# Performance work log

Hardware: AMD Instinct MI355X
Metric: run time of the kernel (lower is better)

## Reference

```python
import jax, jax.numpy as jnp
import numpy as np

B = 512      # batch of scenes
K = 16       # entities (slots) per scene
H = 500      # h == HIDDEN_SIZE (required by fc2 input width 2*HIDDEN_SIZE)
A = 64       # action_size
EPS = 1e-5


def layernorm(x, g, b):
    mu = jnp.mean(x, axis=-1, keepdims=True)
    var = jnp.var(x, axis=-1, keepdims=True)
    return (x - mu) * jax.lax.rsqrt(var + EPS) * g + b


def setup_inputs() -> dict:
    key = jax.random.key(0)
    ks = jax.random.split(key, 40)
    def W(i, shape, scale=0.02):
        return (jax.random.normal(ks[i], shape, dtype=jnp.float32) * scale)
    inp = {
        "state": jax.random.normal(ks[0], (B * K, H), dtype=jnp.float32),
        "actions": jax.random.normal(ks[1], (B, A), dtype=jnp.float32),
        # action path
        "ac_fc1_w": W(2, (A, H)), "ac_fc1_b": jnp.zeros((H,), jnp.float32),
        "ac_ln1_g": jnp.ones((H,), jnp.float32), "ac_ln1_b": jnp.zeros((H,), jnp.float32),
        "ac_fc2_w": W(3, (2 * H, H)), "ac_fc2_b": jnp.zeros((H,), jnp.float32),
        "ac_lnf2_w": W(4, (H, H)), "ac_lnf2_b": jnp.zeros((H,), jnp.float32),  # ac_ln_f2 is a Linear in the source
        "ac_fc3_w": W(5, (2 * H, 1)), "ac_fc3_b": jnp.zeros((1,), jnp.float32),
        # main path
        "fc1_w": W(6, (H, H)), "fc1_b": jnp.zeros((H,), jnp.float32),
        "ln1_g": jnp.ones((H,), jnp.float32), "ln1_b": jnp.zeros((H,), jnp.float32),
        "fc2_w": W(7, (2 * H, H)), "fc2_b": jnp.zeros((H,), jnp.float32),
        "ln2_g": jnp.ones((H,), jnp.float32), "ln2_b": jnp.zeros((H,), jnp.float32),
        "fc3_w": W(8, (H, H)), "fc3_b": jnp.zeros((H,), jnp.float32),
        "ln3_g": jnp.ones((H,), jnp.float32), "ln3_b": jnp.zeros((H,), jnp.float32),
        "fc4_w": W(9, (H, 100)), "fc4_b": jnp.zeros((100,), jnp.float32),
        "ln4_g": jnp.ones((100,), jnp.float32), "ln4_b": jnp.zeros((100,), jnp.float32),
        "fc5_w": W(10, (100, 1)), "fc5_b": jnp.zeros((1,), jnp.float32),
        "fc6_w": W(11, (2 * H, H)), "fc6_b": jnp.zeros((H,), jnp.float32),
        "ln6_g": jnp.ones((H,), jnp.float32), "ln6_b": jnp.zeros((H,), jnp.float32),
    }
    return inp


def reference(state, actions,
              ac_fc1_w, ac_fc1_b, ac_ln1_g, ac_ln1_b,
              ac_fc2_w, ac_fc2_b, ac_lnf2_w, ac_lnf2_b, ac_fc3_w, ac_fc3_b,
              fc1_w, fc1_b, ln1_g, ln1_b,
              fc2_w, fc2_b, ln2_g, ln2_b,
              fc3_w, fc3_b, ln3_g, ln3_b,
              fc4_w, fc4_b, ln4_g, ln4_b,
              fc5_w, fc5_b,
              fc6_w, fc6_b, ln6_g, ln6_b):
    b, k, h, nc = B, K, H, K - 1

    # ---- action_forward (has_action=True) ----
    a = layernorm(actions @ ac_fc1_w + ac_fc1_b, ac_ln1_g, ac_ln1_b)      # [b, h]
    a = jnp.broadcast_to(a[:, None, :], (b, k, h)).reshape(b * k, h)       # repeat over k
    concat_a = jnp.concatenate([state, a], axis=1)                          # [b*k, 2h]
    attention_a = jax.nn.sigmoid(concat_a @ ac_fc3_w + ac_fc3_b)           # [b*k, 1]
    effect = (concat_a @ ac_fc2_w + ac_fc2_b) @ ac_lnf2_w + ac_lnf2_b      # ac_ln_f2 is Linear
    state = effect * attention_a                                            # [b*k, h]

    # ---- per-entity encoder ----
    s1 = jax.nn.relu(layernorm(state @ fc1_w + fc1_b, ln1_g, ln1_b))       # [b*k, h]
    s1r = s1.reshape(b, k, h)

    # ---- all-pairs context gather: for each i, all j != i ----
    idx = np.array([[j for j in range(k) if j != i] for i in range(k)])    # [k, k-1] static
    cs = s1r[:, idx, :]                                                     # [b, k, k-1, h]
    fs = jnp.broadcast_to(s1r[:, :, None, :], (b, k, nc, h))               # [b, k, k-1, h]
    pair = jnp.concatenate([fs, cs], axis=-1).reshape(b * k * nc, 2 * h)   # [b*k*(k-1), 2h]

    # ---- edge MLP ----
    core = jax.nn.relu(layernorm(pair @ fc2_w + fc2_b, ln2_g, ln2_b))      # [b*k*nc, h]
    context = jax.nn.relu(layernorm(core @ fc3_w + fc3_b, ln3_g, ln3_b))
    context = context.reshape(b * k, nc, h)

    # ---- attention-weighted sum aggregation ----
    att = jnp.tanh(layernorm(core @ fc4_w + fc4_b, ln4_g, ln4_b))          # [b*k*nc, 100]
    att = jax.nn.sigmoid(att @ fc5_w + fc5_b).reshape(b * k, nc, 1)
    effect_sum = jnp.sum(context * att, axis=1)                             # [b*k, h]

    # ---- update ----
    total = jnp.concatenate([s1, effect_sum], axis=1)                       # [b*k, 2h]
    h_new = layernorm(total @ fc6_w + fc6_b, ln6_g, ln6_b)                  # [b*k, h]
    return h_new
```

## Files before the change

### kernel.cpp

```cpp
#include <hip/hip_runtime.h>
#include <math.h>


#define EPSF 1e-5f
typedef unsigned short u16;
typedef unsigned int u32;

typedef __bf16 bf16x8 __attribute__((ext_vector_type(8)));
typedef float f32x4 __attribute__((ext_vector_type(4)));
typedef u16 u16x8 __attribute__((ext_vector_type(8)));

__device__ __forceinline__ float bf2f(u16 u) {
  return __builtin_bit_cast(float, (u32)u << 16);
}
__device__ __forceinline__ u16 f2bf(float f) {
  u32 u = __builtin_bit_cast(u32, f);
  return (u16)((u + 0x7FFFu + ((u >> 16) & 1u)) >> 16);
}

#define GLOAD16(g, l) __builtin_amdgcn_global_load_lds( \
    (__attribute__((address_space(1))) u32*)(g), \
    (__attribute__((address_space(3))) u32*)(l), 16, 0, 0)

template <typename TOUT>
__global__ __launch_bounds__(256) void gemm_mfma(
    const u16* __restrict__ A, const u16* __restrict__ A2,
    const u16* __restrict__ Bt,
    const float* __restrict__ bias, const float* __restrict__ rowscale,
    TOUT* __restrict__ C, int M, int Npad, int K, int lda, int khalf)
{
  __shared__ __align__(16) u16 As[2][128 * 64];
  __shared__ __align__(16) u16 Bs[2][64 * 64];
  const int tid = threadIdx.x;
  const int lane = tid & 63, wid = tid >> 6;

  const int ncols = gridDim.x;
  const int nwg = ncols * gridDim.y;
  const int bid = blockIdx.y * ncols + blockIdx.x;
  const int swz = (bid & 7) * (nwg >> 3) + (bid >> 3);
  const size_t row0 = (size_t)(swz / ncols) * 128;
  const size_t col0 = (size_t)(swz % ncols) * 64;

  f32x4 acc[2][4] = {};

  const int s_sub = tid >> 3;
  const int s_chunk = (tid & 7) ^ (s_sub & 7);
  const size_t aoff = (row0 + s_sub) * (size_t)lda + s_chunk * 8;
  const u16* gA = A + aoff;
  const u16* gA2 = A2 ? (A2 + aoff - khalf) : nullptr;
  const u16* gB = Bt + (col0 + s_sub) * (size_t)K + s_chunk * 8;

  const int fr = lane & 15, fq = lane >> 4;
  const int cx0 = fq ^ (fr & 7);
  const int cx1 = (4 + fq) ^ (fr & 7);

  const int nkt = K >> 6;
  int cur = 0;

  {
#pragma unroll
    for (int h = 0; h < 4; ++h)
      GLOAD16(gA + (size_t)h * 32 * lda, &As[0][(h * 256 + tid) * 8]);
#pragma unroll
    for (int h = 0; h < 2; ++h)
      GLOAD16(gB + (size_t)h * 32 * K, &Bs[0][(h * 256 + tid) * 8]);
  }

  for (int kt = 0; kt < nkt; ++kt) {
    if (kt + 1 < nkt) {
      const int kk = (kt + 1) * 64;
      const u16* a = (A2 && kk >= khalf) ? (gA2 + kk) : (gA + kk);
      const u16* b = gB + kk;
#pragma unroll
      for (int h = 0; h < 4; ++h)
        GLOAD16(a + (size_t)h * 32 * lda, &As[cur ^ 1][(h * 256 + tid) * 8]);
#pragma unroll
      for (int h = 0; h < 2; ++h)
        GLOAD16(b + (size_t)h * 32 * K, &Bs[cur ^ 1][(h * 256 + tid) * 8]);
      asm volatile("s_waitcnt vmcnt(6)" ::: "memory");
    } else {
      asm volatile("s_waitcnt vmcnt(0)" ::: "memory");
    }
    __builtin_amdgcn_sched_barrier(0);
    __builtin_amdgcn_s_barrier();
    __builtin_amdgcn_sched_barrier(0);

    const u16* as = As[cur];
    const u16* bs = Bs[cur];
#pragma unroll
    for (int ks = 0; ks < 2; ++ks) {
      const int cx = ks ? cx1 : cx0;
      bf16x8 af[2], bf[4];
#pragma unroll
      for (int m = 0; m < 2; ++m) {
        int row = wid * 32 + m * 16 + fr;
        af[m] = *reinterpret_cast<const bf16x8*>(as + (row * 8 + cx) * 8);
      }
#pragma unroll
      for (int n = 0; n < 4; ++n) {
        int row = n * 16 + fr;
        bf[n] = *reinterpret_cast<const bf16x8*>(bs + (row * 8 + cx) * 8);
      }
#pragma unroll
      for (int m = 0; m < 2; ++m)
#pragma unroll
        for (int n = 0; n < 4; ++n)
          acc[m][n] = __builtin_amdgcn_mfma_f32_16x16x32_bf16(af[m], bf[n], acc[m][n], 0, 0, 0);
    }
    asm volatile("s_waitcnt lgkmcnt(0)" ::: "memory");
    __builtin_amdgcn_sched_barrier(0);
    __builtin_amdgcn_s_barrier();
    __builtin_amdgcn_sched_barrier(0);
    cur ^= 1;
  }

  const int cl = lane & 15, rg = lane >> 4;
#pragma unroll
  for (int m = 0; m < 2; ++m) {
#pragma unroll
    for (int n = 0; n < 4; ++n) {
      size_t col = col0 + n * 16 + cl;
      float bv = bias[col];
#pragma unroll
      for (int r = 0; r < 4; ++r) {
        size_t row = row0 + wid * 32 + m * 16 + rg * 4 + r;
        float v = acc[m][n][r] + bv;
        if (rowscale) v *= rowscale[row];
        if constexpr (sizeof(TOUT) == 2) C[row * Npad + col] = f2bf(v);
        else                             C[row * Npad + col] = v;
      }
    }
  }
}

__global__ __launch_bounds__(256) void gemm128(
    const float* __restrict__ A, const float* __restrict__ B,
    const float* __restrict__ bias, float* __restrict__ C, int M, int N, int K)
{
  __shared__ float As[16][132];
  __shared__ float Bs[16][128];
  const int tid = threadIdx.x;
  const int tx = tid & 15, ty = tid >> 4;
  const int row0 = blockIdx.y * 128, col0 = blockIdx.x * 128;
  float acc[8][8];
#pragma unroll
  for (int i = 0; i < 8; ++i)
#pragma unroll
    for (int j = 0; j < 8; ++j) acc[i][j] = 0.f;

  const int nkt = (K + 15) >> 4;
  for (int kt = 0; kt < nkt; ++kt) {
    const int k0 = kt << 4;
#pragma unroll
    for (int h = 0; h < 2; ++h) {
      int i = tid + h * 256;
      int m = i >> 2, kk = (i & 3) << 2;
      int gm = row0 + m, gk = k0 + kk;
      float4 v = make_float4(0.f, 0.f, 0.f, 0.f);
      if (gm < M && gk < K) v = *reinterpret_cast<const float4*>(A + (size_t)gm * K + gk);
      As[kk + 0][m] = v.x; As[kk + 1][m] = v.y; As[kk + 2][m] = v.z; As[kk + 3][m] = v.w;
    }
#pragma unroll
    for (int h = 0; h < 2; ++h) {
      int i = tid + h * 256;
      int kk = i >> 5, n = (i & 31) << 2;
      int gk = k0 + kk, gn = col0 + n;
      float4 v = make_float4(0.f, 0.f, 0.f, 0.f);
      if (gk < K && gn < N) v = *reinterpret_cast<const float4*>(B + (size_t)gk * N + gn);
      *reinterpret_cast<float4*>(&Bs[kk][n]) = v;
    }
    __syncthreads();
#pragma unroll
    for (int kk = 0; kk < 16; ++kk) {
      float4 a0 = *reinterpret_cast<const float4*>(&As[kk][ty * 4]);
      float4 a1 = *reinterpret_cast<const float4*>(&As[kk][ty * 4 + 64]);
      float4 b0 = *reinterpret_cast<const float4*>(&Bs[kk][tx * 4]);
      float4 b1 = *reinterpret_cast<const float4*>(&Bs[kk][tx * 4 + 64]);
      float av[8] = {a0.x, a0.y, a0.z, a0.w, a1.x, a1.y, a1.z, a1.w};
      float bv[8] = {b0.x, b0.y, b0.z, b0.w, b1.x, b1.y, b1.z, b1.w};
#pragma unroll
      for (int i = 0; i < 8; ++i)
#pragma unroll
        for (int j = 0; j < 8; ++j) acc[i][j] += av[i] * bv[j];
    }
    __syncthreads();
  }
#pragma unroll
  for (int i = 0; i < 8; ++i) {
    int gm = row0 + ty * 4 + ((i >> 2) << 6) + (i & 3);
    if (gm >= M) continue;
#pragma unroll
    for (int j = 0; j < 8; ++j) {
      int gn = col0 + tx * 4 + ((j >> 2) << 6) + (j & 3);
      if (gn < N) C[(size_t)gm * N + gn] = acc[i][j] + bias[gn];
    }
  }
}

template <int ACT, typename TIN, typename TOUT>
__global__ __launch_bounds__(256) void ln_wave4(
    const TIN* __restrict__ X, TOUT* __restrict__ Y,
    const float* __restrict__ g, const float* __restrict__ b,
    int ldx, int ldy)
{
  int w = threadIdx.x >> 6, lane = threadIdx.x & 63;
  int id0 = (blockIdx.x * 4 + w) * 4;
  int k0 = lane * 8;
  float xv[4][8], s[4], s2[4];
#pragma unroll
  for (int r = 0; r < 4; ++r) {
    s[r] = 0.f; s2[r] = 0.f;
    if constexpr (sizeof(TIN) == 2) {
      u16x8 u = *reinterpret_cast<const u16x8*>((const u16*)X + (size_t)(id0 + r) * ldx + k0);
#pragma unroll
      for (int e = 0; e < 8; ++e) xv[r][e] = bf2f(u[e]);
    } else {
      const float* x = (const float*)X + (size_t)(id0 + r) * ldx;
      if (k0 + 8 <= 500) {
        float4 a = *reinterpret_cast<const float4*>(x + k0);
        float4 c = *reinterpret_cast<const float4*>(x + k0 + 4);
        xv[r][0] = a.x; xv[r][1] = a.y; xv[r][2] = a.z; xv[r][3] = a.w;
        xv[r][4] = c.x; xv[r][5] = c.y; xv[r][6] = c.z; xv[r][7] = c.w;
      } else {
#pragma unroll
        for (int e = 0; e < 8; ++e) xv[r][e] = (k0 + e < 500) ? x[k0 + e] : 0.f;
      }
    }
#pragma unroll
    for (int e = 0; e < 8; ++e) { s[r] += xv[r][e]; s2[r] += xv[r][e] * xv[r][e]; }
  }
#pragma unroll
  for (int m = 32; m; m >>= 1)
#pragma unroll
    for (int r = 0; r < 4; ++r) {
      s[r] += __shfl_xor(s[r], m);
      s2[r] += __shfl_xor(s2[r], m);
    }
  float gv[8], bv[8];
#pragma unroll
  for (int e = 0; e < 8; ++e) {
    int k = k0 + e;
    gv[e] = (k < 500) ? g[k] : 0.f;
    bv[e] = (k < 500) ? b[k] : 0.f;
  }
#pragma unroll
  for (int r = 0; r < 4; ++r) {
    float mu = s[r] / 500.f;
    float rstd = rsqrtf(s2[r] / 500.f - mu * mu + EPSF);
    float ov[8];
#pragma unroll
    for (int e = 0; e < 8; ++e) {
      float v = (k0 + e < 500) ? ((xv[r][e] - mu) * rstd * gv[e] + bv[e]) : 0.f;
      if (ACT == 1) v = fmaxf(v, 0.f);
      ov[e] = v;
    }
    if constexpr (sizeof(TOUT) == 2) {
      u16x8 o;
#pragma unroll
      for (int e = 0; e < 8; ++e) o[e] = f2bf(ov[e]);
      *reinterpret_cast<u16x8*>((u16*)Y + (size_t)(id0 + r) * ldy + k0) = o;
    } else {
      float* y = (float*)Y + (size_t)(id0 + r) * ldy;
      if (k0 + 4 <= 500)
        *reinterpret_cast<float4*>(y + k0) = make_float4(ov[0], ov[1], ov[2], ov[3]);
      if (k0 + 8 <= 500)
        *reinterpret_cast<float4*>(y + k0 + 4) = make_float4(ov[4], ov[5], ov[6], ov[7]);
    }
  }
}

__global__ __launch_bounds__(256) void build_concat(
    const float* __restrict__ state, const u16* __restrict__ a, u16* __restrict__ cat)
{
  int r = blockIdx.x, t = threadIdx.x;
  int b = r >> 4;
  u16* c = cat + (size_t)r * 1024;
  if (t < 125) {
    float4 v = *reinterpret_cast<const float4*>(state + (size_t)r * 500 + t * 4);
    ushort4 o; o.x = f2bf(v.x); o.y = f2bf(v.y); o.z = f2bf(v.z); o.w = f2bf(v.w);
    *reinterpret_cast<ushort4*>(c + t * 4) = o;
    *reinterpret_cast<ushort4*>(c + 500 + t * 4) =
        *reinterpret_cast<const ushort4*>(a + (size_t)b * 512 + t * 4);
  }
  if (t < 24) c[1000 + t] = 0;
}

__global__ __launch_bounds__(256) void dot_sig4(
    const u16* __restrict__ cat, const float* __restrict__ w3,
    const float* __restrict__ b3, float* __restrict__ atta)
{
  int w = threadIdx.x >> 6, lane = threadIdx.x & 63;
  int r0 = (blockIdx.x * 4 + w) * 4;
  int k0 = lane * 16;
  float wv[16];
#pragma unroll
  for (int e = 0; e < 16; ++e) wv[e] = (k0 + e < 1000) ? w3[k0 + e] : 0.f;
  float s[4];
#pragma unroll
  for (int r = 0; r < 4; ++r) {
    const u16* x = cat + (size_t)(r0 + r) * 1024 + k0;
    u16x8 u0 = *reinterpret_cast<const u16x8*>(x);
    u16x8 u1 = *reinterpret_cast<const u16x8*>(x + 8);
    float acc = 0.f;
#pragma unroll
    for (int e = 0; e < 8; ++e) acc += bf2f(u0[e]) * wv[e];
#pragma unroll
    for (int e = 0; e < 8; ++e) acc += bf2f(u1[e]) * wv[8 + e];
    s[r] = acc;
  }
#pragma unroll
  for (int m = 32; m; m >>= 1)
#pragma unroll
    for (int r = 0; r < 4; ++r) s[r] += __shfl_xor(s[r], m);
  if (lane == 0) {
#pragma unroll
    for (int r = 0; r < 4; ++r)
      atta[r0 + r] = 1.f / (1.f + expf(-(s[r] + b3[0])));
  }
}

__global__ __launch_bounds__(256) void core_build3(
    const u16* __restrict__ PQ, u16* __restrict__ core,
    const float* __restrict__ g2, const float* __restrict__ b2, int c0)
{
  int w = threadIdx.x >> 6, lane = threadIdx.x & 63;
  int id0 = (blockIdx.x * 4 + w) * 4;
  int k0 = lane * 8;
  u16x8 up[4], uq[4];
#pragma unroll
  for (int r = 0; r < 4; ++r) {
    int id = id0 + r;
    int pp = id / 15, j = id - pp * 15;
    int gp = c0 + pp, i = gp & 15;
    int col = j + (j >= i);
    int r2 = (gp & ~15) | col;
    up[r] = *reinterpret_cast<const u16x8*>(PQ + (size_t)gp * 1024 + k0);
    uq[r] = *reinterpret_cast<const u16x8*>(PQ + (size_t)r2 * 1024 + 512 + k0);
  }
  float xv[4][8], s[4], s2[4];
#pragma unroll
  for (int r = 0; r < 4; ++r) {
    s[r] = 0.f; s2[r] = 0.f;
#pragma unroll
    for (int e = 0; e < 8; ++e) {
      float v = bf2f(up[r][e]) + bf2f(uq[r][e]);
      xv[r][e] = v; s[r] += v; s2[r] += v * v;
    }
  }
#pragma unroll
  for (int m = 32; m; m >>= 1)
#pragma unroll
    for (int r = 0; r < 4; ++r) {
      s[r] += __shfl_xor(s[r], m);
      s2[r] += __shfl_xor(s2[r], m);
    }
  float gv[8], bv[8];
#pragma unroll
  for (int e = 0; e < 8; ++e) {
    int k = k0 + e;
    gv[e] = (k < 500) ? g2[k] : 0.f;
    bv[e] = (k < 500) ? b2[k] : 0.f;
  }
#pragma unroll
  for (int r = 0; r < 4; ++r) {
    float mu = s[r] / 500.f;
    float rstd = rsqrtf(s2[r] / 500.f - mu * mu + EPSF);
    u16x8 o;
#pragma unroll
    for (int e = 0; e < 8; ++e)
      o[e] = (k0 + e < 500) ? f2bf(fmaxf((xv[r][e] - mu) * rstd * gv[e] + bv[e], 0.f)) : (u16)0;
    *reinterpret_cast<u16x8*>(core + (size_t)(id0 + r) * 512 + k0) = o;
  }
}

__global__ __launch_bounds__(256) void chunk_post3(
    const u16* __restrict__ V,
    const float* __restrict__ g3, const float* __restrict__ b3,
    const float* __restrict__ g4, const float* __restrict__ b4,
    const float* __restrict__ w5, const float* __restrict__ b5,
    u16* __restrict__ esum16, int c0)
{
  __shared__ u16 rows[15][512];
  __shared__ float st[15][4];
  int pp = blockIdx.x, t = threadIdx.x;
  int lane = t & 63, w = t >> 6;
  int k0 = lane * 8;
  int kk = lane * 2;

  u16x8 u[4]; ushort2 ua[4];
#pragma unroll
  for (int r = 0; r < 4; ++r) {
    int j = w * 4 + r;
    if (j < 15) {
      const u16* vr = V + (size_t)(pp * 15 + j) * 640;
      u[r] = *reinterpret_cast<const u16x8*>(vr + k0);
      ua[r] = *reinterpret_cast<const ushort2*>(vr + 512 + kk);
    }
  }
  float s[4], s2[4], sa[4], sa2[4], y0[4], y1[4];
#pragma unroll
  for (int r = 0; r < 4; ++r) {
    s[r] = s2[r] = sa[r] = sa2[r] = 0.f; y0[r] = y1[r] = 0.f;
    int j = w * 4 + r;
    if (j < 15) {
#pragma unroll
      for (int e = 0; e < 8; ++e) { float v = bf2f(u[r][e]); s[r] += v; s2[r] += v * v; }
      y0[r] = bf2f(ua[r].x); y1[r] = bf2f(ua[r].y);
      sa[r] = y0[r] + y1[r]; sa2[r] = y0[r] * y0[r] + y1[r] * y1[r];
      *reinterpret_cast<u16x8*>(&rows[j][k0]) = u[r];
    }
  }
#pragma unroll
  for (int m = 32; m; m >>= 1)
#pragma unroll
    for (int r = 0; r < 4; ++r) {
      s[r]   += __shfl_xor(s[r], m);
      s2[r]  += __shfl_xor(s2[r], m);
      sa[r]  += __shfl_xor(sa[r], m);
      sa2[r] += __shfl_xor(sa2[r], m);
    }
  float dv[4];
#pragma unroll
  for (int r = 0; r < 4; ++r) {
    float mu4 = sa[r] / 100.f;
    float rstd4 = rsqrtf(sa2[r] / 100.f - mu4 * mu4 + EPSF);
    float d = 0.f;
    if (kk < 100)     d += tanhf((y0[r] - mu4) * rstd4 * g4[kk] + b4[kk]) * w5[kk];
    if (kk + 1 < 100) d += tanhf((y1[r] - mu4) * rstd4 * g4[kk + 1] + b4[kk + 1]) * w5[kk + 1];
    dv[r] = d;
  }
#pragma unroll
  for (int m = 32; m; m >>= 1)
#pragma unroll
    for (int r = 0; r < 4; ++r) dv[r] += __shfl_xor(dv[r], m);
  if (lane == 0) {
#pragma unroll
    for (int r = 0; r < 4; ++r) {
      int j = w * 4 + r;
      if (j < 15) {
        float mu = s[r] / 500.f;
        st[j][0] = mu;
        st[j][1] = rsqrtf(s2[r] / 500.f - mu * mu + EPSF);
        st[j][2] = 1.f / (1.f + expf(-(dv[r] + b5[0])));
      }
    }
  }
  __syncthreads();

  u16* o = esum16 + (size_t)(c0 + pp) * 512;
  for (int n = t; n < 500; n += 256) {
    float gg = g3[n], bb = b3[n], acc = 0.f;
#pragma unroll
    for (int j = 0; j < 15; ++j) {
      float v = bf2f(rows[j][n]);
      acc += fmaxf((v - st[j][0]) * st[j][1] * gg + bb, 0.f) * st[j][2];
    }
    o[n] = f2bf(acc);
  }
  if (t < 12) o[500 + t] = 0;
}

struct TJob {
  const float* src; u16* dst;
  int K, N, srcLd, ldDst, nOff, kOff, tileBase, tilesX;
};
struct TJobs { TJob j[9]; int total; };

__global__ void pack_weights(TJobs jobs)
{
  __shared__ float tl[32][33];
  int bid = blockIdx.x;
  int ji = 0;
#pragma unroll
  for (int q = 1; q < 9; ++q) if (bid >= jobs.j[q].tileBase) ji = q;
  const TJob& J = jobs.j[ji];
  int t = bid - J.tileBase;
  int bx = t % J.tilesX, by = t / J.tilesX;
  int tx = threadIdx.x, ty = threadIdx.y;
  int k0 = by * 32, n0 = bx * 32;
#pragma unroll
  for (int r = 0; r < 4; ++r) {
    int row = k0 + ty + r * 8;
    if (row < J.K && n0 + tx < J.N) tl[ty + r * 8][tx] = J.src[(size_t)row * J.srcLd + n0 + tx];
  }
  __syncthreads();
#pragma unroll
  for (int r = 0; r < 4; ++r) {
    int n = n0 + ty + r * 8, k = k0 + tx;
    if (n < J.N && k < J.K)
      J.dst[(size_t)(n + J.nOff) * J.ldDst + J.kOff + k] = f2bf(tl[tx][ty + r * 8]);
  }
}

__global__ void pack_biases(
    const float* ac2, const float* lnf2, const float* f1, const float* f2,
    const float* f3, const float* f4, const float* f6,
    float* b_ac2p, float* b_lnf2p, float* b_f1p, float* b2p, float* b34p, float* b_f6p)
{
  int t = threadIdx.x;
  switch (blockIdx.x) {
    case 0: if (t < 512) b_ac2p[t]  = (t < 500) ? ac2[t]  : 0.f; break;
    case 1: if (t < 512) b_lnf2p[t] = (t < 500) ? lnf2[t] : 0.f; break;
    case 2: if (t < 512) b_f1p[t]   = (t < 500) ? f1[t]   : 0.f; break;
    case 3: b2p[t] = (t < 500) ? f2[t] : 0.f; break;
    case 4: if (t < 640) b34p[t] = (t < 500) ? f3[t] : ((t >= 512 && t < 612) ? f4[t - 512] : 0.f); break;
    case 5: if (t < 512) b_f6p[t]   = (t < 500) ? f6[t]   : 0.f; break;
  }
}

extern "C" void kernel_launch(void* const* d_in, const int* in_sizes, int n_in,
                              void* d_out, int out_size, void* d_ws, size_t ws_size,
                              hipStream_t stream)
{
  const float* state    = (const float*)d_in[0];
  const float* actions  = (const float*)d_in[1];
  const float* ac_fc1_w = (const float*)d_in[2];
  const float* ac_fc1_b = (const float*)d_in[3];
  const float* ac_ln1_g = (const float*)d_in[4];
  const float* ac_ln1_b = (const float*)d_in[5];
  const float* ac_fc2_w = (const float*)d_in[6];
  const float* ac_fc2_b = (const float*)d_in[7];
  const float* ac_lnf2_w= (const float*)d_in[8];
  const float* ac_lnf2_b= (const float*)d_in[9];
  const float* ac_fc3_w = (const float*)d_in[10];
  const float* ac_fc3_b = (const float*)d_in[11];
  const float* fc1_w = (const float*)d_in[12];
  const float* fc1_b = (const float*)d_in[13];
  const float* ln1_g = (const float*)d_in[14];
  const float* ln1_b = (const float*)d_in[15];
  const float* fc2_w = (const float*)d_in[16];
  const float* fc2_b = (const float*)d_in[17];
  const float* ln2_g = (const float*)d_in[18];
  const float* ln2_b = (const float*)d_in[19];
  const float* fc3_w = (const float*)d_in[20];
  const float* fc3_b = (const float*)d_in[21];
  const float* ln3_g = (const float*)d_in[22];
  const float* ln3_b = (const float*)d_in[23];
  const float* fc4_w = (const float*)d_in[24];
  const float* fc4_b = (const float*)d_in[25];
  const float* ln4_g = (const float*)d_in[26];
  const float* ln4_b = (const float*)d_in[27];
  const float* fc5_w = (const float*)d_in[28];
  const float* fc5_b = (const float*)d_in[29];
  const float* fc6_w = (const float*)d_in[30];
  const float* fc6_b = (const float*)d_in[31];
  const float* ln6_g = (const float*)d_in[32];
  const float* ln6_b = (const float*)d_in[33];
  float* out = (float*)d_out;

  char* p = (char*)d_ws;
  auto carve = [&](size_t bytes) { char* r = p; p += (bytes + 255) & ~(size_t)255; return r; };
  u16*   cat    = (u16*)  carve(8192ull * 1024 * 2);
  u16*   t1     = (u16*)  carve(8192ull * 512 * 2);
  u16*   s2     = (u16*)  carve(8192ull * 512 * 2);
  u16*   s1     = (u16*)  carve(8192ull * 512 * 2);
  u16*   core   = (u16*)  carve(61440ull * 512 * 2);
  u16*   v      = (u16*)  carve(61440ull * 640 * 2);
  u16*   PQ     = (u16*)  carve(8192ull * 1024 * 2);
  u16*   esum16 = (u16*)  carve(8192ull * 512 * 2);
  u16*   a_buf  = (u16*)  carve(512ull * 512 * 2);
  float* tmp_a  = (float*)carve(512ull * 500 * 4);
  float* att_a  = (float*)carve(8192ull * 4);
  char*  wT0    =         carve(0);
  u16*   ac_fc2T  = (u16*)carve(512ull * 1024 * 2);
  u16*   ac_lnf2T = (u16*)carve(512ull * 512 * 2);
  u16*   fc1T     = (u16*)carve(512ull * 512 * 2);
  u16*   B2T      = (u16*)carve(1024ull * 512 * 2);
  u16*   B34T     = (u16*)carve(640ull * 512 * 2);
  u16*   fc6T     = (u16*)carve(512ull * 1024 * 2);
  size_t wTbytes  = (size_t)((char*)carve(0) - wT0);
  float* b_ac2p  = (float*)carve(512 * 4);
  float* b_lnf2p = (float*)carve(512 * 4);
  float* b_f1p   = (float*)carve(512 * 4);
  float* b2p     = (float*)carve(1024 * 4);
  float* b34p    = (float*)carve(640 * 4);
  float* b_f6p   = (float*)carve(512 * 4);

  dim3 blk(256);
  dim3 tblk(32, 8);

  hipMemsetAsync(wT0, 0, wTbytes, stream);
  TJobs jobs;
  int base = 0;
  auto addjob = [&](int idx, const float* src, u16* dst, int K, int N, int srcLd,
                    int ldDst, int nOff, int kOff) {
    int tx = (N + 31) / 32, ty = (K + 31) / 32;
    jobs.j[idx] = {src, dst, K, N, srcLd, ldDst, nOff, kOff, base, tx};
    base += tx * ty;
  };
  addjob(0, ac_fc2_w,         ac_fc2T,  1000, 500, 500, 1024, 0, 0);
  addjob(1, ac_lnf2_w,        ac_lnf2T,  500, 500, 500,  512, 0, 0);
  addjob(2, fc1_w,            fc1T,      500, 500, 500,  512, 0, 0);
  addjob(3, fc2_w,            B2T,       500, 500, 500,  512, 0, 0);
  addjob(4, fc2_w + 250000,   B2T,       500, 500, 500,  512, 512, 0);
  addjob(5, fc3_w,            B34T,      500, 500, 500,  512, 0, 0);
  addjob(6, fc4_w,            B34T,      500, 100, 100,  512, 512, 0);
  addjob(7, fc6_w,            fc6T,      500, 500, 500, 1024, 0, 0);
  addjob(8, fc6_w + 250000,   fc6T,      500, 500, 500, 1024, 0, 512);
  jobs.total = base;
  pack_weights<<<base, tblk, 0, stream>>>(jobs);
  pack_biases<<<6, 1024, 0, stream>>>(ac_fc2_b, ac_lnf2_b, fc1_b, fc2_b, fc3_b, fc4_b, fc6_b,
                                      b_ac2p, b_lnf2p, b_f1p, b2p, b34p, b_f6p);

  gemm128<<<dim3(4, 4), blk, 0, stream>>>(actions, ac_fc1_w, ac_fc1_b, tmp_a, 512, 500, 64);
  ln_wave4<0, float, u16><<<32, blk, 0, stream>>>(tmp_a, a_buf, ac_ln1_g, ac_ln1_b, 500, 512);
  build_concat<<<8192, blk, 0, stream>>>(state, a_buf, cat);

  gemm_mfma<u16><<<dim3(8, 64), blk, 0, stream>>>(cat, nullptr, ac_fc2T, b_ac2p, nullptr,
                                                  t1, 8192, 512, 1024, 1024, 0);
  dot_sig4<<<512, blk, 0, stream>>>(cat, ac_fc3_w, ac_fc3_b, att_a);
  gemm_mfma<u16><<<dim3(8, 64), blk, 0, stream>>>(t1, nullptr, ac_lnf2T, b_lnf2p, att_a,
                                                  s2, 8192, 512, 512, 512, 0);
  gemm_mfma<u16><<<dim3(8, 64), blk, 0, stream>>>(s2, nullptr, fc1T, b_f1p, nullptr,
                                                  t1, 8192, 512, 512, 512, 0);
  ln_wave4<1, u16, u16><<<512, blk, 0, stream>>>(t1, s1, ln1_g, ln1_b, 512, 512);
  gemm_mfma<u16><<<dim3(16, 64), blk, 0, stream>>>(s1, nullptr, B2T, b2p, nullptr,
                                                   PQ, 8192, 1024, 512, 512, 0);

  for (int c = 0; c < 2; ++c) {
    int c0 = c * 4096;
    core_build3<<<3840, blk, 0, stream>>>(PQ, core, ln2_g, ln2_b, c0);
    gemm_mfma<u16><<<dim3(10, 480), blk, 0, stream>>>(core, nullptr, B34T, b34p, nullptr,
                                                      v, 61440, 640, 512, 512, 0);
    chunk_post3<<<4096, blk, 0, stream>>>(v, ln3_g, ln3_b, ln4_g, ln4_b, fc5_w, fc5_b,
                                          esum16, c0);
  }

  gemm_mfma<u16><<<dim3(8, 64), blk, 0, stream>>>(s1, esum16, fc6T, b_f6p, nullptr,
                                                  t1, 8192, 512, 1024, 512, 512);
  ln_wave4<0, u16, float><<<512, blk, 0, stream>>>(t1, out, ln6_g, ln6_b, 512, 500);
}
```

Measured before the change: 428.2 us.

## Add 128x128 GEMM tile variant, halve edge chunk size, swizzle block order

Templates the MFMA GEMM on the N-tile width and adds a 128x128 tile, where each wave computes a 64x64 sub-tile, for the PQ GEMM and the large edge GEMM. This raises arithmetic intensity per LDS load. The edge pipeline now runs in four chunks of 2048 scenes-slots instead of two, so the core and v intermediates are half the size and more likely to stay cache-resident. The core_build3 and chunk_post3 kernels also get a block-index swizzle. The trade-offs are more accumulator registers, which can lower occupancy, and twice as many kernel launches.

```diff
diff --git a/kernel.cpp b/kernel.cpp
--- a/kernel.cpp
+++ b/kernel.cpp
@@ -22,26 +22,30 @@
     (__attribute__((address_space(1))) u32*)(g), \
     (__attribute__((address_space(3))) u32*)(l), 16, 0, 0)
 
-template <typename TOUT>
+template <typename TOUT, int BN>
 __global__ __launch_bounds__(256) void gemm_mfma(
     const u16* __restrict__ A, const u16* __restrict__ A2,
     const u16* __restrict__ Bt,
     const float* __restrict__ bias, const float* __restrict__ rowscale,
     TOUT* __restrict__ C, int M, int Npad, int K, int lda, int khalf)
 {
+  constexpr int MR = (BN == 64) ? 2 : 4;
+  constexpr int NLOADS = 4 + BN / 32;
   __shared__ __align__(16) u16 As[2][128 * 64];
-  __shared__ __align__(16) u16 Bs[2][64 * 64];
+  __shared__ __align__(16) u16 Bs[2][BN * 64];
   const int tid = threadIdx.x;
   const int lane = tid & 63, wid = tid >> 6;
+  const int arow_base = (BN == 64) ? wid * 32 : (wid >> 1) * 64;
+  const int bcol_base = (BN == 64) ? 0 : (wid & 1) * 64;
 
   const int ncols = gridDim.x;
   const int nwg = ncols * gridDim.y;
   const int bid = blockIdx.y * ncols + blockIdx.x;
   const int swz = (bid & 7) * (nwg >> 3) + (bid >> 3);
   const size_t row0 = (size_t)(swz / ncols) * 128;
-  const size_t col0 = (size_t)(swz % ncols) * 64;
-
-  f32x4 acc[2][4] = {};
+  const size_t col0 = (size_t)(swz % ncols) * BN;
+
+  f32x4 acc[MR][4] = {};
 
   const int s_sub = tid >> 3;
   const int s_chunk = (tid & 7) ^ (s_sub & 7);
@@ -62,7 +66,7 @@
     for (int h = 0; h < 4; ++h)
       GLOAD16(gA + (size_t)h * 32 * lda, &As[0][(h * 256 + tid) * 8]);
 #pragma unroll
-    for (int h = 0; h < 2; ++h)
+    for (int h = 0; h < BN / 32; ++h)
       GLOAD16(gB + (size_t)h * 32 * K, &Bs[0][(h * 256 + tid) * 8]);
   }
 
@@ -75,9 +79,12 @@
       for (int h = 0; h < 4; ++h)
         GLOAD16(a + (size_t)h * 32 * lda, &As[cur ^ 1][(h * 256 + tid) * 8]);
 #pragma unroll
-      for (int h = 0; h < 2; ++h)
+      for (int h = 0; h < BN / 32; ++h)
         GLOAD16(b + (size_t)h * 32 * K, &Bs[cur ^ 1][(h * 256 + tid) * 8]);
-      asm volatile("s_waitcnt vmcnt(6)" ::: "memory");
+      if constexpr (NLOADS == 6)
+        asm volatile("s_waitcnt vmcnt(6)" ::: "memory");
+      else
+        asm volatile("s_waitcnt vmcnt(8)" ::: "memory");
     } else {
       asm volatile("s_waitcnt vmcnt(0)" ::: "memory");
     }
@@ -90,19 +97,19 @@
 #pragma unroll
     for (int ks = 0; ks < 2; ++ks) {
       const int cx = ks ? cx1 : cx0;
-      bf16x8 af[2], bf[4];
-#pragma unroll
-      for (int m = 0; m < 2; ++m) {
-        int row = wid * 32 + m * 16 + fr;
+      bf16x8 af[MR], bf[4];
+#pragma unroll
+      for (int m = 0; m < MR; ++m) {
+        int row = arow_base + m * 16 + fr;
         af[m] = *reinterpret_cast<const bf16x8*>(as + (row * 8 + cx) * 8);
       }
 #pragma unroll
       for (int n = 0; n < 4; ++n) {
-        int row = n * 16 + fr;
+        int row = bcol_base + n * 16 + fr;
         bf[n] = *reinterpret_cast<const bf16x8*>(bs + (row * 8 + cx) * 8);
       }
 #pragma unroll
-      for (int m = 0; m < 2; ++m)
+      for (int m = 0; m < MR; ++m)
 #pragma unroll
         for (int n = 0; n < 4; ++n)
           acc[m][n] = __builtin_amdgcn_mfma_f32_16x16x32_bf16(af[m], bf[n], acc[m][n], 0, 0, 0);
@@ -116,14 +123,14 @@
 
   const int cl = lane & 15, rg = lane >> 4;
 #pragma unroll
-  for (int m = 0; m < 2; ++m) {
+  for (int m = 0; m < MR; ++m) {
 #pragma unroll
     for (int n = 0; n < 4; ++n) {
-      size_t col = col0 + n * 16 + cl;
+      size_t col = col0 + bcol_base + n * 16 + cl;
       float bv = bias[col];
 #pragma unroll
       for (int r = 0; r < 4; ++r) {
-        size_t row = row0 + wid * 32 + m * 16 + rg * 4 + r;
+        size_t row = row0 + arow_base + m * 16 + rg * 4 + r;
         float v = acc[m][n][r] + bv;
         if (rowscale) v *= rowscale[row];
         if constexpr (sizeof(TOUT) == 2) C[row * Npad + col] = f2bf(v);
@@ -324,7 +331,9 @@
     const float* __restrict__ g2, const float* __restrict__ b2, int c0)
 {
   int w = threadIdx.x >> 6, lane = threadIdx.x & 63;
-  int id0 = (blockIdx.x * 4 + w) * 4;
+  int bid = blockIdx.x;
+  int rb = (bid & 7) * (gridDim.x >> 3) + (bid >> 3);
+  int id0 = (rb * 4 + w) * 4;
   int k0 = lane * 8;
   u16x8 up[4], uq[4];
 #pragma unroll
@@ -382,7 +391,8 @@
 {
   __shared__ u16 rows[15][512];
   __shared__ float st[15][4];
-  int pp = blockIdx.x, t = threadIdx.x;
+  int bid = blockIdx.x, t = threadIdx.x;
+  int pp = (bid & 7) * (gridDim.x >> 3) + (bid >> 3);
   int lane = t & 63, w = t >> 6;
   int k0 = lane * 8;
   int kk = lane * 2;
@@ -554,8 +564,8 @@
   u16*   t1     = (u16*)  carve(8192ull * 512 * 2);
   u16*   s2     = (u16*)  carve(8192ull * 512 * 2);
   u16*   s1     = (u16*)  carve(8192ull * 512 * 2);
-  u16*   core   = (u16*)  carve(61440ull * 512 * 2);
-  u16*   v      = (u16*)  carve(61440ull * 640 * 2);
+  u16*   core   = (u16*)  carve(30720ull * 512 * 2);
+  u16*   v      = (u16*)  carve(30720ull * 640 * 2);
   u16*   PQ     = (u16*)  carve(8192ull * 1024 * 2);
   u16*   esum16 = (u16*)  carve(8192ull * 512 * 2);
   u16*   a_buf  = (u16*)  carve(512ull * 512 * 2);
@@ -606,27 +616,27 @@
   ln_wave4<0, float, u16><<<32, blk, 0, stream>>>(tmp_a, a_buf, ac_ln1_g, ac_ln1_b, 500, 512);
   build_concat<<<8192, blk, 0, stream>>>(state, a_buf, cat);
 
-  gemm_mfma<u16><<<dim3(8, 64), blk, 0, stream>>>(cat, nullptr, ac_fc2T, b_ac2p, nullptr,
-                                                  t1, 8192, 512, 1024, 1024, 0);
+  gemm_mfma<u16, 64><<<dim3(8, 64), blk, 0, stream>>>(cat, nullptr, ac_fc2T, b_ac2p, nullptr,
+                                                      t1, 8192, 512, 1024, 1024, 0);
   dot_sig4<<<512, blk, 0, stream>>>(cat, ac_fc3_w, ac_fc3_b, att_a);
-  gemm_mfma<u16><<<dim3(8, 64), blk, 0, stream>>>(t1, nullptr, ac_lnf2T, b_lnf2p, att_a,
-                                                  s2, 8192, 512, 512, 512, 0);
-  gemm_mfma<u16><<<dim3(8, 64), blk, 0, stream>>>(s2, nullptr, fc1T, b_f1p, nullptr,
-                                                  t1, 8192, 512, 512, 512, 0);
+  gemm_mfma<u16, 64><<<dim3(8, 64), blk, 0, stream>>>(t1, nullptr, ac_lnf2T, b_lnf2p, att_a,
+                                                      s2, 8192, 512, 512, 512, 0);
+  gemm_mfma<u16, 64><<<dim3(8, 64), blk, 0, stream>>>(s2, nullptr, fc1T, b_f1p, nullptr,
+                                                      t1, 8192, 512, 512, 512, 0);
   ln_wave4<1, u16, u16><<<512, blk, 0, stream>>>(t1, s1, ln1_g, ln1_b, 512, 512);
-  gemm_mfma<u16><<<dim3(16, 64), blk, 0, stream>>>(s1, nullptr, B2T, b2p, nullptr,
-                                                   PQ, 8192, 1024, 512, 512, 0);
-
-  for (int c = 0; c < 2; ++c) {
-    int c0 = c * 4096;
-    core_build3<<<3840, blk, 0, stream>>>(PQ, core, ln2_g, ln2_b, c0);
-    gemm_mfma<u16><<<dim3(10, 480), blk, 0, stream>>>(core, nullptr, B34T, b34p, nullptr,
-                                                      v, 61440, 640, 512, 512, 0);
-    chunk_post3<<<4096, blk, 0, stream>>>(v, ln3_g, ln3_b, ln4_g, ln4_b, fc5_w, fc5_b,
+  gemm_mfma<u16, 128><<<dim3(8, 64), blk, 0, stream>>>(s1, nullptr, B2T, b2p, nullptr,
+                                                       PQ, 8192, 1024, 512, 512, 0);
+
+  for (int c = 0; c < 4; ++c) {
+    int c0 = c * 2048;
+    core_build3<<<1920, blk, 0, stream>>>(PQ, core, ln2_g, ln2_b, c0);
+    gemm_mfma<u16, 128><<<dim3(5, 240), blk, 0, stream>>>(core, nullptr, B34T, b34p, nullptr,
+                                                          v, 30720, 640, 512, 512, 0);
+    chunk_post3<<<2048, blk, 0, stream>>>(v, ln3_g, ln3_b, ln4_g, ln4_b, fc5_w, fc5_b,
                                           esum16, c0);
   }
 
-  gemm_mfma<u16><<<dim3(8, 64), blk, 0, stream>>>(s1, esum16, fc6T, b_f6p, nullptr,
-                                                  t1, 8192, 512, 1024, 512, 512);
+  gemm_mfma<u16, 64><<<dim3(8, 64), blk, 0, stream>>>(s1, esum16, fc6T, b_f6p, nullptr,
+                                                      t1, 8192, 512, 1024, 512, 512);
   ln_wave4<0, u16, float><<<512, blk, 0, stream>>>(t1, out, ln6_g, ln6_b, 512, 500);
 }
```

Measured after the change: 473.0 us. +10.5%, slower.
